# Optimization experiments

Measured on AMD Instinct MI355X. Metric: run time of the kernel, lower is better.

## Reference

```python
import jax, jax.numpy as jnp
import numpy as np
import math

D_MODEL = 256
D_HEAD = 64
N_LEVELS = 2
N_HEADS = 8
N_POINTS = 4
SHAPES = [(100, 176), (50, 88)]  # (H, W) per level -> Len_in = 22000


def setup_inputs() -> dict:
    key = jax.random.key(0)
    ks = jax.random.split(key, 8)
    N, Lq = 2, 22000
    Len_in = sum(h * w for h, w in SHAPES)
    query = jax.random.normal(ks[0], (N, Lq, D_MODEL), jnp.float32)
    input_flatten = jax.random.normal(ks[1], (N, Len_in, D_MODEL), jnp.float32)
    input_spatial_shapes = jnp.array(SHAPES, jnp.int32)
    input_level_start_index = jnp.array([0, SHAPES[0][0] * SHAPES[0][1]], jnp.int32)
    # reference points in pixel units (original divides them by offset_normalizer)
    norm = jnp.array([[w, h] for (h, w) in SHAPES], jnp.float32)  # [L,2] as (x=W, y=H)
    reference_points = jax.random.uniform(ks[2], (N, Lq, N_LEVELS, 2), jnp.float32) * norm[None, None]
    xav = lambda k, shp: jax.random.normal(k, shp, jnp.float32) * math.sqrt(2.0 / (shp[0] + shp[1]))
    Wv = xav(ks[3], (D_MODEL, N_HEADS * D_HEAD))
    bv = jnp.zeros((N_HEADS * D_HEAD,), jnp.float32)
    Woff = jax.random.normal(ks[4], (D_MODEL, N_HEADS * N_LEVELS * N_POINTS * 2), jnp.float32) * 0.01
    # grid-init bias exactly as in _reset_parameters
    thetas = jnp.arange(N_HEADS, dtype=jnp.float32) * (2.0 * math.pi / N_HEADS)
    grid = jnp.stack([jnp.cos(thetas), jnp.sin(thetas)], -1)
    grid = grid / jnp.max(jnp.abs(grid), -1, keepdims=True)
    grid = jnp.tile(grid[:, None, None, :], (1, N_LEVELS, N_POINTS, 1))
    grid = grid * jnp.arange(1, N_POINTS + 1, dtype=jnp.float32)[None, None, :, None]
    boff = grid.reshape(-1)
    Wattn = jax.random.normal(ks[5], (D_MODEL, N_HEADS * N_LEVELS * N_POINTS), jnp.float32) * 0.01
    battn = jnp.zeros((N_HEADS * N_LEVELS * N_POINTS,), jnp.float32)
    Wo = xav(ks[6], (N_HEADS * D_HEAD, D_MODEL))
    bo = jnp.zeros((D_MODEL,), jnp.float32)
    return dict(query=query, reference_points=reference_points, input_flatten=input_flatten,
                Wv=Wv, bv=bv, Woff=Woff, boff=boff, Wattn=Wattn, battn=battn, Wo=Wo, bo=bo,
                input_spatial_shapes=input_spatial_shapes,
                input_level_start_index=input_level_start_index)


def ms_deform_core(value, sampling_locations, attention_weights, shapes_np):
    # value: [N, Len_in, H, D]; sampling_locations: [N, Lq, H, L, P, 2] in [0,1]
    # attention_weights: [N, Lq, H, L, P]
    N, _, Hh_, D = value.shape
    Lq = sampling_locations.shape[1]
    P = sampling_locations.shape[4]
    out = jnp.zeros((N, Lq, Hh_, D), value.dtype)
    start = 0
    for lvl, (Hl, Wl) in enumerate(shapes_np):
        Hl, Wl = int(Hl), int(Wl)
        v = value[:, start:start + Hl * Wl]  # [N, Hl*Wl, H, D]
        start += Hl * Wl
        loc = sampling_locations[:, :, :, lvl]  # [N, Lq, H, P, 2]
        # grid_sample align_corners=False convention
        x = loc[..., 0] * Wl - 0.5
        y = loc[..., 1] * Hl - 0.5
        x0 = jnp.floor(x); y0 = jnp.floor(y)
        fx = x - x0; fy = y - y0
        x0i = x0.astype(jnp.int32); y0i = y0.astype(jnp.int32)
        acc = jnp.zeros((N, Lq, P, Hh_, D), value.dtype)
        for dx, dy, w in ((0, 0, (1 - fx) * (1 - fy)), (1, 0, fx * (1 - fy)),
                          (0, 1, (1 - fx) * fy), (1, 1, fx * fy)):
            xi = x0i + dx; yi = y0i + dy
            valid = (xi >= 0) & (xi < Wl) & (yi >= 0) & (yi < Hl)
            idx = jnp.clip(yi, 0, Hl - 1) * Wl + jnp.clip(xi, 0, Wl - 1)  # [N, Lq, H, P]
            idx_t = idx.transpose(0, 1, 3, 2).reshape(N, Lq * P, Hh_, 1)
            g = jnp.take_along_axis(v, idx_t, axis=1).reshape(N, Lq, P, Hh_, D)
            wz = jnp.where(valid, w, 0.0)  # zero padding outside
            acc = acc + g * wz.transpose(0, 1, 3, 2)[..., None]
        out = out + jnp.einsum('nqphd,nqhp->nqhd', acc, attention_weights[:, :, :, lvl])
    return out.reshape(N, Lq, Hh_ * D)


def reference(query, reference_points, input_flatten, Wv, bv, Woff, boff, Wattn, battn, Wo, bo,
              input_spatial_shapes, input_level_start_index):
    shapes_np = np.asarray(input_spatial_shapes)
    N, Lq, _ = query.shape
    value = (input_flatten @ Wv + bv).reshape(N, -1, N_HEADS, D_HEAD)
    off = (query @ Woff + boff).reshape(N, Lq, N_HEADS, N_LEVELS, N_POINTS, 2)
    aw = jax.nn.softmax((query @ Wattn + battn).reshape(N, Lq, N_HEADS, N_LEVELS * N_POINTS), -1)
    aw = aw.reshape(N, Lq, N_HEADS, N_LEVELS, N_POINTS)
    normalizer = jnp.stack([shapes_np[:, 1], shapes_np[:, 0]], -1).astype(jnp.float32)  # [L,2] (W,H)
    loc = (reference_points[:, :, None, :, None, :] + off) / normalizer[None, None, None, :, None, :]
    out = ms_deform_core(value, loc, aw, shapes_np)
    return out @ Wo + bo
```

## Files before the change

### kernel.cpp

```cpp
#include <hip/hip_runtime.h>

#define LQ        22000
#define LEN_IN    22000
#define NB        2

typedef _Float16 half8 __attribute__((ext_vector_type(8)));
typedef _Float16 half4 __attribute__((ext_vector_type(4)));
typedef _Float16 half2 __attribute__((ext_vector_type(2)));
typedef float    floatx4 __attribute__((ext_vector_type(4)));

__global__ __launch_bounds__(256) void prep_kernel(
    const float* __restrict__ Wv, const float* __restrict__ Woff,
    const float* __restrict__ Wattn, const float* __restrict__ Wo,
    const float* __restrict__ boff, const float* __restrict__ battn,
    _Float16* __restrict__ WvT, _Float16* __restrict__ WofT,
    _Float16* __restrict__ WoT, float* __restrict__ biascat)
{
    const int i = blockIdx.x * 256 + threadIdx.x;
    if (i < 131072) {
        int k = i >> 9, n = i & 511;
        WvT[n * 256 + k] = (_Float16)Wv[i];
    } else if (i < 163840) {
        int j = i - 131072; int k = j >> 7, n = j & 127;
        WofT[n * 256 + k] = (_Float16)Woff[j];
    } else if (i < 180224) {
        int j = i - 163840; int k = j >> 6, n = j & 63;
        WofT[(128 + n) * 256 + k] = (_Float16)Wattn[j];
    } else if (i < 311296) {
        int j = i - 180224; int k = j >> 8, n = j & 255;
        WoT[n * 512 + k] = (_Float16)Wo[j];
    } else if (i < 311488) {
        int j = i - 311296;
        biascat[j] = (j < 128) ? boff[j] : battn[j - 128];
    }
}

template<bool A_F32, bool OUT_F16>
__global__ __launch_bounds__(256) void gemm_kernel(
    const void* __restrict__ Aq,
    const _Float16* __restrict__ BT,
    const float* __restrict__ bias,
    void* __restrict__ C,
    int M, int N, int K)
{
    __shared__ __align__(16) _Float16 sA[128][72];
    __shared__ __align__(16) _Float16 sB[64][72];

    const int t  = threadIdx.x;
    const int m0 = blockIdx.x * 128;
    const int n0 = blockIdx.y * 64;

    const int w    = t >> 6;
    const int lane = t & 63;
    const int wm   = w * 32;
    const int lrow = lane & 15;
    const int lk   = (lane >> 4) * 8;

    const int ar = t >> 1;
    const int ah = (t & 1) * 32;
    const int br = t >> 2;
    const int bs = (t & 3) * 16;

    floatx4 acc[2][4] = {};

    for (int k0 = 0; k0 < K; k0 += 64) {
        const int arow = m0 + ar;
        if constexpr (A_F32) {
            const float4* src = reinterpret_cast<const float4*>(
                (const float*)Aq + (size_t)arow * K + k0 + ah);
            half4* dst = reinterpret_cast<half4*>(&sA[ar][ah]);
            #pragma unroll
            for (int j = 0; j < 8; ++j) {
                float4 v = {0.f, 0.f, 0.f, 0.f};
                if (arow < M) v = src[j];
                half4 h;
                h[0] = (_Float16)v.x; h[1] = (_Float16)v.y;
                h[2] = (_Float16)v.z; h[3] = (_Float16)v.w;
                dst[j] = h;
            }
        } else {
            int4 v0 = {0,0,0,0}, v1 = v0, v2 = v0, v3 = v0;
            if (arow < M) {
                const int4* src = reinterpret_cast<const int4*>(
                    (const _Float16*)Aq + (size_t)arow * K + k0 + ah);
                v0 = src[0]; v1 = src[1]; v2 = src[2]; v3 = src[3];
            }
            int4* dst = reinterpret_cast<int4*>(&sA[ar][ah]);
            dst[0] = v0; dst[1] = v1; dst[2] = v2; dst[3] = v3;
        }
        {
            const int4* src = reinterpret_cast<const int4*>(BT + (size_t)(n0 + br) * K + k0 + bs);
            int4* dst = reinterpret_cast<int4*>(&sB[br][bs]);
            dst[0] = src[0]; dst[1] = src[1];
        }
        __syncthreads();

        #pragma unroll
        for (int kb = 0; kb < 2; ++kb) {
            const int ko = kb * 32 + lk;
            half8 a0 = *reinterpret_cast<const half8*>(&sA[wm + lrow][ko]);
            half8 a1 = *reinterpret_cast<const half8*>(&sA[wm + 16 + lrow][ko]);
            half8 b0 = *reinterpret_cast<const half8*>(&sB[lrow][ko]);
            half8 b1 = *reinterpret_cast<const half8*>(&sB[16 + lrow][ko]);
            half8 b2 = *reinterpret_cast<const half8*>(&sB[32 + lrow][ko]);
            half8 b3 = *reinterpret_cast<const half8*>(&sB[48 + lrow][ko]);
            acc[0][0] = __builtin_amdgcn_mfma_f32_16x16x32_f16(a0, b0, acc[0][0], 0, 0, 0);
            acc[0][1] = __builtin_amdgcn_mfma_f32_16x16x32_f16(a0, b1, acc[0][1], 0, 0, 0);
            acc[0][2] = __builtin_amdgcn_mfma_f32_16x16x32_f16(a0, b2, acc[0][2], 0, 0, 0);
            acc[0][3] = __builtin_amdgcn_mfma_f32_16x16x32_f16(a0, b3, acc[0][3], 0, 0, 0);
            acc[1][0] = __builtin_amdgcn_mfma_f32_16x16x32_f16(a1, b0, acc[1][0], 0, 0, 0);
            acc[1][1] = __builtin_amdgcn_mfma_f32_16x16x32_f16(a1, b1, acc[1][1], 0, 0, 0);
            acc[1][2] = __builtin_amdgcn_mfma_f32_16x16x32_f16(a1, b2, acc[1][2], 0, 0, 0);
            acc[1][3] = __builtin_amdgcn_mfma_f32_16x16x32_f16(a1, b3, acc[1][3], 0, 0, 0);
        }
        __syncthreads();
    }

    const int crow = (lane >> 4) * 4;
    const int ccol = lane & 15;
    #pragma unroll
    for (int fm = 0; fm < 2; ++fm) {
        #pragma unroll
        for (int fn = 0; fn < 4; ++fn) {
            const int col = n0 + fn * 16 + ccol;
            const float b = bias[col];
            #pragma unroll
            for (int r2 = 0; r2 < 4; ++r2) {
                const int row = m0 + wm + fm * 16 + crow + r2;
                if (row < M) {
                    const float val = acc[fm][fn][r2] + b;
                    if (OUT_F16)
                        ((_Float16*)C)[(size_t)row * N + col] = (_Float16)val;
                    else
                        ((float*)C)[(size_t)row * N + col] = val;
                }
            }
        }
    }
}

__global__ __launch_bounds__(256) void sampler_kernel(
    const _Float16* __restrict__ value,
    const _Float16* __restrict__ logits,
    const float*    __restrict__ refp,
    _Float16* __restrict__ sampled)
{
    const int t    = threadIdx.x;
    const int wq   = t >> 6;
    const int lane = t & 63;
    const int q    = blockIdx.x * 4 + wq;

    __shared__ __align__(16) int4  s_idx[4][72];
    __shared__ __align__(16) uint4 s_w[4][72];

    {
        const int s = lane;
        const int h = s >> 3;
        const int l = (s >> 2) & 1;
        const int p = s & 3;
        const _Float16* lg = logits + (size_t)q * 192;

        float logit[8];
        float m = -1e30f;
        #pragma unroll
        for (int j = 0; j < 8; ++j) {
            logit[j] = (float)lg[128 + h * 8 + j];
            m = fmaxf(m, logit[j]);
        }
        float den = 0.f;
        #pragma unroll
        for (int j = 0; j < 8; ++j) den += __expf(logit[j] - m);
        const float aw = __expf(logit[l * 4 + p] - m) / den;

        const int Hl = l ? 50 : 100;
        const int Wl = l ? 88 : 176;
        const int st = l ? 17600 : 0;
        const float rx = refp[q * 4 + l * 2 + 0];
        const float ry = refp[q * 4 + l * 2 + 1];
        const float ox = (float)lg[h * 16 + l * 8 + p * 2 + 0];
        const float oy = (float)lg[h * 16 + l * 8 + p * 2 + 1];

        const float x = rx + ox - 0.5f;
        const float y = ry + oy - 0.5f;
        const float x0f = floorf(x), y0f = floorf(y);
        const float fx = x - x0f, fy = y - y0f;
        const int x0 = (int)x0f, y0 = (int)y0f;

        int4  iv;
        uint4 wv;
        #pragma unroll
        for (int c = 0; c < 4; ++c) {
            const int xi = x0 + (c & 1);
            const int yi = y0 + (c >> 1);
            const bool valid = (xi >= 0) & (xi < Wl) & (yi >= 0) & (yi < Hl);
            const float wb = ((c & 1) ? fx : 1.f - fx) * ((c >> 1) ? fy : 1.f - fy);
            const float wz = valid ? wb * aw : 0.f;
            const int xc = min(max(xi, 0), Wl - 1);
            const int yc = min(max(yi, 0), Hl - 1);
            iv[c] = st + yc * Wl + xc;
            union { half2 h; unsigned int u; } cv;
            cv.h[0] = (_Float16)wz; cv.h[1] = cv.h[0];
            wv[c] = cv.u;
        }
        const int slot = h * 9 + (l * 4 + p);
        s_idx[wq][slot] = iv;
        s_w[wq][slot]   = wv;
    }
    __syncthreads();

    const int h  = lane >> 3;
    const int d8 = (lane & 7) * 8;
    const _Float16* vbase = value + h * 64 + d8;

    half2 acc0 = {0.f16, 0.f16}, acc1 = acc0, acc2 = acc0, acc3 = acc0;
    #pragma unroll
    for (int s8 = 0; s8 < 8; ++s8) {
        const int4  iv = s_idx[wq][h * 9 + s8];
        const uint4 wv = s_w[wq][h * 9 + s8];
        #pragma unroll
        for (int c = 0; c < 4; ++c) {
            const half8 v = *reinterpret_cast<const half8*>(vbase + (size_t)iv[c] * 512);
            union { unsigned int u; half2 h; } cv; cv.u = wv[c];
            const half2 wh = cv.h;
            half2 p0; p0[0] = v[0]; p0[1] = v[1];
            half2 p1; p1[0] = v[2]; p1[1] = v[3];
            half2 p2; p2[0] = v[4]; p2[1] = v[5];
            half2 p3; p3[0] = v[6]; p3[1] = v[7];
            acc0 += p0 * wh;
            acc1 += p1 * wh;
            acc2 += p2 * wh;
            acc3 += p3 * wh;
        }
    }
    half8 o;
    o[0] = acc0[0]; o[1] = acc0[1];
    o[2] = acc1[0]; o[3] = acc1[1];
    o[4] = acc2[0]; o[5] = acc2[1];
    o[6] = acc3[0]; o[7] = acc3[1];
    *reinterpret_cast<half8*>(sampled + (size_t)q * 512 + h * 64 + d8) = o;
}

extern "C" void kernel_launch(void* const* d_in, const int* in_sizes, int n_in,
                              void* d_out, int out_size, void* d_ws, size_t ws_size,
                              hipStream_t stream)
{
    const float* query  = (const float*)d_in[0];
    const float* refp   = (const float*)d_in[1];
    const float* inflat = (const float*)d_in[2];
    const float* Wv     = (const float*)d_in[3];
    const float* bv     = (const float*)d_in[4];
    const float* Woff   = (const float*)d_in[5];
    const float* boff   = (const float*)d_in[6];
    const float* Wattn  = (const float*)d_in[7];
    const float* battn  = (const float*)d_in[8];
    const float* Wo     = (const float*)d_in[9];
    const float* bo     = (const float*)d_in[10];
    float* out = (float*)d_out;

    char* ws = (char*)d_ws;
    size_t off = 0;
    auto take = [&](size_t bytes) { char* p = ws + off; off = (off + bytes + 255) & ~(size_t)255; return p; };
    _Float16* WvT     = (_Float16*)take(512 * 256 * 2);
    _Float16* WofT    = (_Float16*)take(192 * 256 * 2);
    _Float16* WoT     = (_Float16*)take(256 * 512 * 2);
    float*    biascat = (float*)   take(192 * 4);
    _Float16* value   = (_Float16*)take((size_t)NB * LEN_IN * 512 * 2);
    _Float16* logits  = (_Float16*)take((size_t)NB * LQ * 192 * 2);
    _Float16* sampled = (_Float16*)take((size_t)LQ * 512 * 2);

    prep_kernel<<<(311488 + 255) / 256, 256, 0, stream>>>(
        Wv, Woff, Wattn, Wo, boff, battn, WvT, WofT, WoT, biascat);

    const int M2   = NB * LQ;
    const int MG2  = (M2 + 127) / 128;
    const int MG1  = (LQ + 127) / 128;

    gemm_kernel<true, true><<<dim3(MG2, 8), 256, 0, stream>>>(
        inflat, WvT, bv, value, M2, 512, 256);
    gemm_kernel<true, true><<<dim3(MG2, 3), 256, 0, stream>>>(
        query, WofT, biascat, logits, M2, 192, 256);

    for (int n = 0; n < NB; ++n) {
        sampler_kernel<<<LQ / 4, 256, 0, stream>>>(
            value  + (size_t)n * LEN_IN * 512,
            logits + (size_t)n * LQ * 192,
            refp   + (size_t)n * LQ * 4,
            sampled);
        gemm_kernel<false, false><<<dim3(MG1, 4), 256, 0, stream>>>(
            sampled, WoT, bo, out + (size_t)n * LQ * 256, LQ, 256, 512);
    }
}
```

Baseline: 395.6 us.

## Pre-convert inputs to fp16, register-prefetch GEMM tiles, process batches sequentially

Separate kernels now convert the fp32 input and query to fp16 before the GEMMs. The GEMM is templated on N-tile width and K, with 128-wide tiles for the value and output projections. Each tile is loaded into registers and the next is prefetched while the MFMAs run, so the second barrier is gone. The per-batch loop now covers all stages, shrinking workspace so buffers stay cache-resident, with the sampled buffer aliasing the input fp16 buffer. The trade-off is extra conversion passes and more kernel launches against better reuse per block and overlap of global loads.

```diff
diff --git a/kernel.cpp b/kernel.cpp
--- a/kernel.cpp
+++ b/kernel.cpp
@@ -35,98 +35,108 @@
     }
 }
 
-template<bool A_F32, bool OUT_F16>
+__global__ void f32_to_f16_kernel(const float* __restrict__ src,
+                                  _Float16* __restrict__ dst, int n4)
+{
+    int i = blockIdx.x * blockDim.x + threadIdx.x;
+    const int stride = gridDim.x * blockDim.x;
+    for (; i < n4; i += stride) {
+        float4 v = reinterpret_cast<const float4*>(src)[i];
+        half4 h;
+        h[0] = (_Float16)v.x; h[1] = (_Float16)v.y;
+        h[2] = (_Float16)v.z; h[3] = (_Float16)v.w;
+        reinterpret_cast<half4*>(dst)[i] = h;
+    }
+}
+
+template<int BN, int K, bool OUT_F16>
 __global__ __launch_bounds__(256) void gemm_kernel(
-    const void* __restrict__ Aq,
+    const _Float16* __restrict__ A,
     const _Float16* __restrict__ BT,
     const float* __restrict__ bias,
     void* __restrict__ C,
-    int M, int N, int K)
-{
+    int M, int N)
+{
+    constexpr int T  = K / 64;
+    constexpr int RB = BN / 32;
+    constexpr int FM = (BN == 128) ? 4 : 2;
+
     __shared__ __align__(16) _Float16 sA[128][72];
-    __shared__ __align__(16) _Float16 sB[64][72];
-
-    const int t  = threadIdx.x;
-    const int m0 = blockIdx.x * 128;
-    const int n0 = blockIdx.y * 64;
-
+    __shared__ __align__(16) _Float16 sB[BN][72];
+
+    const int t    = threadIdx.x;
+    const int m0   = blockIdx.x * 128;
+    const int n0   = blockIdx.y * BN;
     const int w    = t >> 6;
     const int lane = t & 63;
-    const int wm   = w * 32;
+    const int wr   = (BN == 128) ? (w >> 1) * 64 : w * 32;
+    const int wc   = (BN == 128) ? (w & 1) * 64 : 0;
     const int lrow = lane & 15;
     const int lk   = (lane >> 4) * 8;
-
-    const int ar = t >> 1;
-    const int ah = (t & 1) * 32;
-    const int br = t >> 2;
-    const int bs = (t & 3) * 16;
-
-    floatx4 acc[2][4] = {};
-
-    for (int k0 = 0; k0 < K; k0 += 64) {
-        const int arow = m0 + ar;
-        if constexpr (A_F32) {
-            const float4* src = reinterpret_cast<const float4*>(
-                (const float*)Aq + (size_t)arow * K + k0 + ah);
-            half4* dst = reinterpret_cast<half4*>(&sA[ar][ah]);
-            #pragma unroll
-            for (int j = 0; j < 8; ++j) {
-                float4 v = {0.f, 0.f, 0.f, 0.f};
-                if (arow < M) v = src[j];
-                half4 h;
-                h[0] = (_Float16)v.x; h[1] = (_Float16)v.y;
-                h[2] = (_Float16)v.z; h[3] = (_Float16)v.w;
-                dst[j] = h;
-            }
-        } else {
-            int4 v0 = {0,0,0,0}, v1 = v0, v2 = v0, v3 = v0;
-            if (arow < M) {
-                const int4* src = reinterpret_cast<const int4*>(
-                    (const _Float16*)Aq + (size_t)arow * K + k0 + ah);
-                v0 = src[0]; v1 = src[1]; v2 = src[2]; v3 = src[3];
-            }
-            int4* dst = reinterpret_cast<int4*>(&sA[ar][ah]);
-            dst[0] = v0; dst[1] = v1; dst[2] = v2; dst[3] = v3;
-        }
-        {
-            const int4* src = reinterpret_cast<const int4*>(BT + (size_t)(n0 + br) * K + k0 + bs);
-            int4* dst = reinterpret_cast<int4*>(&sB[br][bs]);
-            dst[0] = src[0]; dst[1] = src[1];
-        }
+    const int srow = t >> 3;
+    const int scol = (t & 7) * 8;
+
+    int4 areg[4], breg[RB];
+    auto load_tile = [&](int k0) {
+        #pragma unroll
+        for (int j = 0; j < 4; ++j) {
+            const int r = m0 + srow + 32 * j;
+            int4 v = {0, 0, 0, 0};
+            if (r < M)
+                v = *reinterpret_cast<const int4*>(A + (size_t)r * K + k0 + scol);
+            areg[j] = v;
+        }
+        #pragma unroll
+        for (int j = 0; j < RB; ++j)
+            breg[j] = *reinterpret_cast<const int4*>(
+                BT + (size_t)(n0 + srow + 32 * j) * K + k0 + scol);
+    };
+
+    floatx4 acc[FM][4] = {};
+
+    load_tile(0);
+    #pragma unroll
+    for (int it = 0; it < T; ++it) {
         __syncthreads();
+        #pragma unroll
+        for (int j = 0; j < 4; ++j)
+            *reinterpret_cast<int4*>(&sA[srow + 32 * j][scol]) = areg[j];
+        #pragma unroll
+        for (int j = 0; j < RB; ++j)
+            *reinterpret_cast<int4*>(&sB[srow + 32 * j][scol]) = breg[j];
+        __syncthreads();
+        if (it + 1 < T) load_tile((it + 1) * 64);
 
         #pragma unroll
         for (int kb = 0; kb < 2; ++kb) {
             const int ko = kb * 32 + lk;
-            half8 a0 = *reinterpret_cast<const half8*>(&sA[wm + lrow][ko]);
-            half8 a1 = *reinterpret_cast<const half8*>(&sA[wm + 16 + lrow][ko]);
-            half8 b0 = *reinterpret_cast<const half8*>(&sB[lrow][ko]);
-            half8 b1 = *reinterpret_cast<const half8*>(&sB[16 + lrow][ko]);
-            half8 b2 = *reinterpret_cast<const half8*>(&sB[32 + lrow][ko]);
-            half8 b3 = *reinterpret_cast<const half8*>(&sB[48 + lrow][ko]);
-            acc[0][0] = __builtin_amdgcn_mfma_f32_16x16x32_f16(a0, b0, acc[0][0], 0, 0, 0);
-            acc[0][1] = __builtin_amdgcn_mfma_f32_16x16x32_f16(a0, b1, acc[0][1], 0, 0, 0);
-            acc[0][2] = __builtin_amdgcn_mfma_f32_16x16x32_f16(a0, b2, acc[0][2], 0, 0, 0);
-            acc[0][3] = __builtin_amdgcn_mfma_f32_16x16x32_f16(a0, b3, acc[0][3], 0, 0, 0);
-            acc[1][0] = __builtin_amdgcn_mfma_f32_16x16x32_f16(a1, b0, acc[1][0], 0, 0, 0);
-            acc[1][1] = __builtin_amdgcn_mfma_f32_16x16x32_f16(a1, b1, acc[1][1], 0, 0, 0);
-            acc[1][2] = __builtin_amdgcn_mfma_f32_16x16x32_f16(a1, b2, acc[1][2], 0, 0, 0);
-            acc[1][3] = __builtin_amdgcn_mfma_f32_16x16x32_f16(a1, b3, acc[1][3], 0, 0, 0);
-        }
-        __syncthreads();
+            half8 a[FM], b[4];
+            #pragma unroll
+            for (int fm = 0; fm < FM; ++fm)
+                a[fm] = *reinterpret_cast<const half8*>(&sA[wr + fm * 16 + lrow][ko]);
+            #pragma unroll
+            for (int fn = 0; fn < 4; ++fn)
+                b[fn] = *reinterpret_cast<const half8*>(&sB[wc + fn * 16 + lrow][ko]);
+            #pragma unroll
+            for (int fm = 0; fm < FM; ++fm)
+                #pragma unroll
+                for (int fn = 0; fn < 4; ++fn)
+                    acc[fm][fn] = __builtin_amdgcn_mfma_f32_16x16x32_f16(
+                        a[fm], b[fn], acc[fm][fn], 0, 0, 0);
+        }
     }
 
     const int crow = (lane >> 4) * 4;
     const int ccol = lane & 15;
     #pragma unroll
-    for (int fm = 0; fm < 2; ++fm) {
+    for (int fm = 0; fm < FM; ++fm) {
         #pragma unroll
         for (int fn = 0; fn < 4; ++fn) {
-            const int col = n0 + fn * 16 + ccol;
+            const int col = n0 + wc + fn * 16 + ccol;
             const float b = bias[col];
             #pragma unroll
             for (int r2 = 0; r2 < 4; ++r2) {
-                const int row = m0 + wm + fm * 16 + crow + r2;
+                const int row = m0 + wr + fm * 16 + crow + r2;
                 if (row < M) {
                     const float val = acc[fm][fn][r2] + b;
                     if (OUT_F16)
@@ -264,29 +274,34 @@
     _Float16* WofT    = (_Float16*)take(192 * 256 * 2);
     _Float16* WoT     = (_Float16*)take(256 * 512 * 2);
     float*    biascat = (float*)   take(192 * 4);
-    _Float16* value   = (_Float16*)take((size_t)NB * LEN_IN * 512 * 2);
-    _Float16* logits  = (_Float16*)take((size_t)NB * LQ * 192 * 2);
-    _Float16* sampled = (_Float16*)take((size_t)LQ * 512 * 2);
+    _Float16* inbf    = (_Float16*)take((size_t)LEN_IN * 256 * 2);
+    _Float16* qbf     = (_Float16*)take((size_t)LQ * 256 * 2);
+    _Float16* value   = (_Float16*)take((size_t)LEN_IN * 512 * 2);
+    _Float16* logits  = (_Float16*)take((size_t)LQ * 192 * 2);
+    _Float16* sampled = inbf;
 
     prep_kernel<<<(311488 + 255) / 256, 256, 0, stream>>>(
         Wv, Woff, Wattn, Wo, boff, battn, WvT, WofT, WoT, biascat);
 
-    const int M2   = NB * LQ;
-    const int MG2  = (M2 + 127) / 128;
-    const int MG1  = (LQ + 127) / 128;
-
-    gemm_kernel<true, true><<<dim3(MG2, 8), 256, 0, stream>>>(
-        inflat, WvT, bv, value, M2, 512, 256);
-    gemm_kernel<true, true><<<dim3(MG2, 3), 256, 0, stream>>>(
-        query, WofT, biascat, logits, M2, 192, 256);
+    const int MG = (LQ + 127) / 128;
 
     for (int n = 0; n < NB; ++n) {
-        sampler_kernel<<<LQ / 4, 256, 0, stream>>>(
-            value  + (size_t)n * LEN_IN * 512,
-            logits + (size_t)n * LQ * 192,
-            refp   + (size_t)n * LQ * 4,
-            sampled);
-        gemm_kernel<false, false><<<dim3(MG1, 4), 256, 0, stream>>>(
-            sampled, WoT, bo, out + (size_t)n * LQ * 256, LQ, 256, 512);
-    }
-}
+        const float* in_n  = inflat + (size_t)n * LEN_IN * 256;
+        const float* q_n   = query  + (size_t)n * LQ * 256;
+        const float* rp_n  = refp   + (size_t)n * LQ * 4;
+        float*       out_n = out    + (size_t)n * LQ * 256;
+
+        f32_to_f16_kernel<<<1024, 256, 0, stream>>>(in_n, inbf, LEN_IN * 256 / 4);
+        f32_to_f16_kernel<<<1024, 256, 0, stream>>>(q_n, qbf, LQ * 256 / 4);
+
+        gemm_kernel<128, 256, true><<<dim3(MG, 4), 256, 0, stream>>>(
+            inbf, WvT, bv, value, LEN_IN, 512);
+        gemm_kernel<64, 256, true><<<dim3(MG, 3), 256, 0, stream>>>(
+            qbf, WofT, biascat, logits, LQ, 192);
+
+        sampler_kernel<<<LQ / 4, 256, 0, stream>>>(value, logits, rp_n, sampled);
+
+        gemm_kernel<128, 512, false><<<dim3(MG, 2), 256, 0, stream>>>(
+            sampled, WoT, bo, out_n, LQ, 256);
+    }
+}
```

After: 425.0 us. +7.4%, slower.
